# Kernel optimization log

Hardware: AMD Instinct MI355X
Metric: run time of the kernel (lower is better)

Reference implementation:

```python
import jax, jax.numpy as jnp
import numpy as np

E_DIM = 1024
HID = 4096
H = (2 * HID) // 3  # floor(2*hidden/3) = 2730
NUM_EXPERTS = 8
TOP_K = 2
LN_EPS = 1e-5


def setup_inputs() -> dict:
    key = jax.random.key(0)
    ks = jax.random.split(key, 10)
    B, T, P = 2, 8, 256
    s_in = 1.0 / np.sqrt(E_DIM)
    s_h = 1.0 / np.sqrt(H)
    return {
        "x": jax.random.normal(ks[0], (B, T, P, E_DIM), jnp.float32),
        "Wr": jax.random.normal(ks[1], (NUM_EXPERTS, E_DIM), jnp.float32) * s_in,
        "Wv": jax.random.normal(ks[2], (NUM_EXPERTS, E_DIM, H), jnp.float32) * s_in,
        "bv": jax.random.normal(ks[3], (NUM_EXPERTS, H), jnp.float32) * 0.01,
        "Wg": jax.random.normal(ks[4], (NUM_EXPERTS, E_DIM, H), jnp.float32) * s_in,
        "bg": jax.random.normal(ks[5], (NUM_EXPERTS, H), jnp.float32) * 0.01,
        "Wo": jax.random.normal(ks[6], (NUM_EXPERTS, H, E_DIM), jnp.float32) * s_h,
        "bo": jax.random.normal(ks[7], (NUM_EXPERTS, E_DIM), jnp.float32) * 0.01,
        "ln_g": jnp.ones((E_DIM,), jnp.float32),
        "ln_b": jnp.zeros((E_DIM,), jnp.float32),
    }


def reference(x, Wr, Wv, bv, Wg, bg, Wo, bo, ln_g, ln_b):
    B, T, P, E = x.shape
    flat = x.reshape(-1, E)          # [N, E]
    N = flat.shape[0]

    # router: top-k logits -> softmax combine weights
    logits = flat @ Wr.T                              # [N, C]
    tk_vals, tk_idx = jax.lax.top_k(logits, TOP_K)    # [N, K]
    tk_w = jax.nn.softmax(tk_vals, axis=-1)           # [N, K]

    # dense combine-weight matrix: zero for non-routed experts
    comb = jnp.zeros((N, NUM_EXPERTS), flat.dtype)
    comb = comb.at[jnp.arange(N)[:, None], tk_idx].add(tk_w)  # [N, C]

    # all experts over all tokens (masked combine makes this exact)
    hv = jnp.einsum('ne,ceh->cnh', flat, Wv) + bv[:, None, :]  # [C, N, H]
    hg = jnp.einsum('ne,ceh->cnh', flat, Wg) + bg[:, None, :]
    h = jax.nn.silu(hv) * hg                                   # SwiGLU
    oe = jnp.einsum('cnh,che->cne', h, Wo) + bo[:, None, :]    # [C, N, E]
    out = jnp.einsum('cne,nc->ne', oe, comb)                   # weighted combine

    # residual + LayerNorm (AdaptiveNormalizer with no conditioning)
    y = x + out.reshape(B, T, P, E)
    mu = jnp.mean(y, axis=-1, keepdims=True)
    var = jnp.mean((y - mu) ** 2, axis=-1, keepdims=True)
    return ln_g * (y - mu) * jax.lax.rsqrt(var + LN_EPS) + ln_b
```

## Files before the change

kernel.cpp:

```cpp
#include <hip/hip_runtime.h>
#include <hip/hip_bf16.h>

#define E_DIM 1024
#define HDIM  2730
#define HP    2816
#define NEXP  8
#define NTOK  4096
#define NPAIR 8192
#define NSLOT 72
#define LN_EPS 1e-5f

typedef __attribute__((ext_vector_type(8))) short  short8;
typedef __attribute__((ext_vector_type(4))) short  short4v;
typedef __attribute__((ext_vector_type(4))) float  floatx4;
typedef __attribute__((ext_vector_type(4))) int    intx4;

__device__ __forceinline__ __hip_bfloat16 f2bf(float f) { return __float2bfloat16(f); }

__device__ __forceinline__ void gload16(const __hip_bfloat16* g, __hip_bfloat16* l) {
  __builtin_amdgcn_global_load_lds(
      (const __attribute__((address_space(1))) void*)(g),
      (__attribute__((address_space(3))) void*)(l), 16, 0, 0);
}

__global__ __launch_bounds__(256) void router_k(const float* __restrict__ x,
    const float* __restrict__ Wr, int* __restrict__ counts,
    int* __restrict__ tk_idx, float* __restrict__ tk_w) {
  int wid = threadIdx.x >> 6, lane = threadIdx.x & 63;
  int t = blockIdx.x * 4 + wid;
  const float* xr = x + (size_t)t * E_DIM;
  float xv[16];
#pragma unroll
  for (int i = 0; i < 16; ++i) xv[i] = xr[lane + 64 * i];
  float lg[8];
#pragma unroll
  for (int e = 0; e < 8; ++e) {
    const float* wr = Wr + e * E_DIM;
    float a = 0.f;
#pragma unroll
    for (int i = 0; i < 16; ++i) a += xv[i] * wr[lane + 64 * i];
#pragma unroll
    for (int o = 32; o; o >>= 1) a += __shfl_xor(a, o, 64);
    lg[e] = a;
  }
  if (lane == 0) {
    int i0 = 0; float l0 = lg[0];
#pragma unroll
    for (int e = 1; e < 8; ++e) if (lg[e] > l0) { l0 = lg[e]; i0 = e; }
    int i1 = -1; float l1 = -1e30f;
#pragma unroll
    for (int e = 0; e < 8; ++e) if (e != i0 && lg[e] > l1) { l1 = lg[e]; i1 = e; }
    float w0 = 1.f / (1.f + __expf(l1 - l0));
    atomicAdd(&counts[i0], 1);
    atomicAdd(&counts[i1], 1);
    tk_idx[2 * t]     = i0;  tk_idx[2 * t + 1] = i1;
    tk_w[2 * t]       = w0;  tk_w[2 * t + 1]   = 1.f - w0;
  }
}

__global__ void offsets_k(const int* __restrict__ counts, int* __restrict__ offsets,
                          int* __restrict__ cursor,
                          int* __restrict__ slot_e, int* __restrict__ slot_m0) {
  if (threadIdx.x == 0) {
    int off = 0, s = 0;
    for (int e = 0; e < NEXP; ++e) {
      offsets[e] = off; cursor[e] = off;
      for (int m0 = 0; m0 < counts[e]; m0 += 128) { slot_e[s] = e; slot_m0[s] = m0; ++s; }
      off += counts[e];
    }
    for (; s < NSLOT; ++s) { slot_e[s] = -1; slot_m0[s] = 0; }
  }
}

__global__ __launch_bounds__(256) void scatter_k(const int* __restrict__ tk_idx,
    const float* __restrict__ tk_w, int* __restrict__ cursor,
    int* __restrict__ pair_token, float* __restrict__ pair_w, int* __restrict__ pair_pos) {
  int t = blockIdx.x * 256 + threadIdx.x;
#pragma unroll
  for (int k = 0; k < 2; ++k) {
    int e = tk_idx[2 * t + k];
    int pos = atomicAdd(&cursor[e], 1);
    pair_token[pos] = t;
    pair_w[pos] = tk_w[2 * t + k];
    pair_pos[2 * t + k] = pos;
  }
}

__global__ __launch_bounds__(256) void gatherx_k(const float* __restrict__ x,
    const int* __restrict__ pair_token, __hip_bfloat16* __restrict__ xs) {
  int p = blockIdx.x;
  int t = pair_token[p];
  const float* src = x + (size_t)t * E_DIM;
  __hip_bfloat16* dst = xs + (size_t)p * E_DIM;
  int i = threadIdx.x * 4;
  floatx4 v = *(const floatx4*)(src + i);
  union { __hip_bfloat16 h[4]; short4v s; } u;
#pragma unroll
  for (int j = 0; j < 4; ++j) u.h[j] = f2bf(v[j]);
  *(short4v*)(dst + i) = u.s;
}

__global__ __launch_bounds__(256) void tcvt_k(const float* __restrict__ in,
    __hip_bfloat16* __restrict__ out, int R, int C, int outRS,
    size_t inExpStride, size_t outExpStride) {
  __shared__ float tile[64 * 65];
  int e = blockIdx.z;
  const float* ip = in + inExpStride * e;
  __hip_bfloat16* op = out + outExpStride * e;
  int c0 = blockIdx.x * 64, r0 = blockIdx.y * 64;
#pragma unroll
  for (int i = 0; i < 16; ++i) {
    int idx = i * 256 + threadIdx.x;
    int rr = idx >> 6, cc = idx & 63;
    int gr = r0 + rr, gc = c0 + cc;
    tile[rr * 65 + cc] = (gr < R && gc < C) ? ip[(size_t)gr * C + gc] : 0.f;
  }
  __syncthreads();
#pragma unroll
  for (int i = 0; i < 2; ++i) {
    int idx = i * 256 + threadIdx.x;
    int cc = idx >> 3, rb = (idx & 7) * 8;
    union { __hip_bfloat16 h[8]; intx4 v; } u;
#pragma unroll
    for (int j = 0; j < 8; ++j) u.h[j] = f2bf(tile[(rb + j) * 65 + cc]);
    *(intx4*)(op + (size_t)(c0 + cc) * outRS + (r0 + rb)) = u.v;
  }
}

__global__ __launch_bounds__(256, 2) void gemm1_k(
    const __hip_bfloat16* __restrict__ xs,
    const int* __restrict__ counts, const int* __restrict__ offsets,
    const int* __restrict__ slot_e, const int* __restrict__ slot_m0,
    const float* __restrict__ bv, const float* __restrict__ bg,
    const __hip_bfloat16* __restrict__ WvT, const __hip_bfloat16* __restrict__ WgT,
    __hip_bfloat16* __restrict__ h) {
  int slot = blockIdx.y;
  int e = slot_e[slot];
  if (e < 0) return;
  int m0 = slot_m0[slot];
  int Me = counts[e], off = offsets[e];
  int n0 = blockIdx.x * 128;

  __shared__ __align__(16) __hip_bfloat16 sA[128 * 64];
  __shared__ __align__(16) __hip_bfloat16 sBv[128 * 64];
  __shared__ __align__(16) __hip_bfloat16 sBg[128 * 64];

  int tid = threadIdx.x;
  int wid = tid >> 6, lane = tid & 63;
  int wm = wid >> 1, wn = wid & 1;
  int q = lane >> 4, r = lane & 15;
  int key = r & 7;

  int sw[2];
  sw[0] = ((q ^ key) << 3);
  sw[1] = (((4 + q) ^ key) << 3);
  int arow = (wm * 64 + r) * 64;
  int brow = (wn * 64 + r) * 64;

  int srow8  = lane >> 3;
  int schunk = (lane & 7) ^ srow8;
  const __hip_bfloat16* gA0 = xs + (size_t)(off + m0 + wid * 8 + srow8) * E_DIM + schunk * 8;
  size_t wb = (size_t)e * ((size_t)HP * E_DIM);
  size_t browoff = wb + (size_t)(n0 + wid * 8 + srow8) * E_DIM + schunk * 8;
  const __hip_bfloat16* gBv0 = WvT + browoff;
  const __hip_bfloat16* gBg0 = WgT + browoff;
  __hip_bfloat16* lA0  = sA  + wid * 512;
  __hip_bfloat16* lBv0 = sBv + wid * 512;
  __hip_bfloat16* lBg0 = sBg + wid * 512;

  floatx4 accv[4][4], accg[4][4];
  floatx4 zz = {0.f, 0.f, 0.f, 0.f};
#pragma unroll
  for (int mi = 0; mi < 4; ++mi)
#pragma unroll
    for (int ni = 0; ni < 4; ++ni) { accv[mi][ni] = zz; accg[mi][ni] = zz; }

  for (int kt = 0; kt < E_DIM / 64; ++kt) {
    int ko = kt * 64;
#pragma unroll
    for (int i = 0; i < 4; ++i) gload16(gA0  + ko + (size_t)i * 32 * E_DIM, lA0  + i * 2048);
#pragma unroll
    for (int i = 0; i < 4; ++i) gload16(gBv0 + ko + (size_t)i * 32 * E_DIM, lBv0 + i * 2048);
#pragma unroll
    for (int i = 0; i < 4; ++i) gload16(gBg0 + ko + (size_t)i * 32 * E_DIM, lBg0 + i * 2048);
    __syncthreads();
#pragma unroll
    for (int s = 0; s < 2; ++s) {
      short8 av[4];
#pragma unroll
      for (int mi = 0; mi < 4; ++mi)
        av[mi] = *(const short8*)(sA + arow + mi * 16 * 64 + sw[s]);
#pragma unroll
      for (int ni = 0; ni < 4; ++ni) {
        short8 b8v = *(const short8*)(sBv + brow + ni * 16 * 64 + sw[s]);
        short8 b8g = *(const short8*)(sBg + brow + ni * 16 * 64 + sw[s]);
#pragma unroll
        for (int mi = 0; mi < 4; ++mi) {
          accv[mi][ni] = __builtin_amdgcn_mfma_f32_16x16x32_bf16(av[mi], b8v, accv[mi][ni], 0, 0, 0);
          accg[mi][ni] = __builtin_amdgcn_mfma_f32_16x16x32_bf16(av[mi], b8g, accg[mi][ni], 0, 0, 0);
        }
      }
    }
    __syncthreads();
  }

  float bvv[4], bgv[4];
#pragma unroll
  for (int ni = 0; ni < 4; ++ni) {
    int n = n0 + wn * 64 + ni * 16 + r;
    bvv[ni] = (n < HDIM) ? bv[e * HDIM + n] : 0.f;
    bgv[ni] = (n < HDIM) ? bg[e * HDIM + n] : 0.f;
  }
#pragma unroll
  for (int mi = 0; mi < 4; ++mi) {
#pragma unroll
    for (int rr = 0; rr < 4; ++rr) {
      int m_loc = wm * 64 + mi * 16 + q * 4 + rr;
      int m = m0 + m_loc;
      if (m >= Me) continue;
      size_t hrow = (size_t)(off + m) * HP;
#pragma unroll
      for (int ni = 0; ni < 4; ++ni) {
        int n = n0 + wn * 64 + ni * 16 + r;
        float hv = accv[mi][ni][rr] + bvv[ni];
        float hg = accg[mi][ni][rr] + bgv[ni];
        float sgm = 1.f / (1.f + __expf(-hv));
        h[hrow + n] = f2bf(hv * sgm * hg);
      }
    }
  }
}

__global__ __launch_bounds__(256) void gemm2_k(
    const __hip_bfloat16* __restrict__ hb,
    const int* __restrict__ counts, const int* __restrict__ offsets,
    const int* __restrict__ slot_e, const int* __restrict__ slot_m0,
    const float* __restrict__ bo,
    const __hip_bfloat16* __restrict__ WoT,
    float* __restrict__ pout) {
  int slot = blockIdx.y;
  int e = slot_e[slot];
  if (e < 0) return;
  int m0 = slot_m0[slot];
  int Me = counts[e], off = offsets[e];
  int n0 = blockIdx.x * 128;

  __shared__ __align__(16) __hip_bfloat16 sA[128 * 64];
  __shared__ __align__(16) __hip_bfloat16 sB[128 * 64];

  int tid = threadIdx.x;
  int wid = tid >> 6, lane = tid & 63;
  int wm = wid >> 1, wn = wid & 1;
  int q = lane >> 4, r = lane & 15;
  int key = r & 7;

  int sw[2];
  sw[0] = ((q ^ key) << 3);
  sw[1] = (((4 + q) ^ key) << 3);
  int arow = (wm * 64 + r) * 64;
  int brow = (wn * 64 + r) * 64;

  int srow8  = lane >> 3;
  int schunk = (lane & 7) ^ srow8;
  const __hip_bfloat16* gA0 = hb + (size_t)(off + m0 + wid * 8 + srow8) * HP + schunk * 8;
  const __hip_bfloat16* gB0 = WoT + (size_t)e * ((size_t)E_DIM * HP) +
                              (size_t)(n0 + wid * 8 + srow8) * HP + schunk * 8;
  __hip_bfloat16* lA0 = sA + wid * 512;
  __hip_bfloat16* lB0 = sB + wid * 512;

  floatx4 acc[4][4];
  floatx4 zz = {0.f, 0.f, 0.f, 0.f};
#pragma unroll
  for (int mi = 0; mi < 4; ++mi)
#pragma unroll
    for (int ni = 0; ni < 4; ++ni) acc[mi][ni] = zz;

  for (int kt = 0; kt < HP / 64; ++kt) {
    int ko = kt * 64;
#pragma unroll
    for (int i = 0; i < 4; ++i) gload16(gA0 + ko + (size_t)i * 32 * HP, lA0 + i * 2048);
#pragma unroll
    for (int i = 0; i < 4; ++i) gload16(gB0 + ko + (size_t)i * 32 * HP, lB0 + i * 2048);
    __syncthreads();
#pragma unroll
    for (int s = 0; s < 2; ++s) {
      short8 av[4];
#pragma unroll
      for (int mi = 0; mi < 4; ++mi)
        av[mi] = *(const short8*)(sA + arow + mi * 16 * 64 + sw[s]);
#pragma unroll
      for (int ni = 0; ni < 4; ++ni) {
        short8 b8 = *(const short8*)(sB + brow + ni * 16 * 64 + sw[s]);
#pragma unroll
        for (int mi = 0; mi < 4; ++mi)
          acc[mi][ni] = __builtin_amdgcn_mfma_f32_16x16x32_bf16(av[mi], b8, acc[mi][ni], 0, 0, 0);
      }
    }
    __syncthreads();
  }

#pragma unroll
  for (int mi = 0; mi < 4; ++mi) {
#pragma unroll
    for (int rr = 0; rr < 4; ++rr) {
      int m_loc = wm * 64 + mi * 16 + q * 4 + rr;
      int m = m0 + m_loc;
      if (m >= Me) continue;
      size_t orow = (size_t)(off + m) * E_DIM;
#pragma unroll
      for (int ni = 0; ni < 4; ++ni) {
        int n = n0 + wn * 64 + ni * 16 + r;
        pout[orow + n] = acc[mi][ni][rr] + bo[e * E_DIM + n];
      }
    }
  }
}

__global__ __launch_bounds__(256) void ln_k(const float* __restrict__ x,
    const float* __restrict__ pout, const int* __restrict__ pair_pos,
    const float* __restrict__ pair_w, const float* __restrict__ ln_g,
    const float* __restrict__ ln_b, float* __restrict__ out) {
  int t = blockIdx.x, tid = threadIdx.x;
  int p0 = pair_pos[2 * t], p1 = pair_pos[2 * t + 1];
  float w0 = pair_w[p0], w1 = pair_w[p1];
  const float* xr = x + (size_t)t * E_DIM;
  const float* r0 = pout + (size_t)p0 * E_DIM;
  const float* r1 = pout + (size_t)p1 * E_DIM;
  float y[4];
  float s = 0.f, ss = 0.f;
#pragma unroll
  for (int i = 0; i < 4; ++i) {
    int e = tid + 256 * i;
    y[i] = xr[e] + w0 * r0[e] + w1 * r1[e];
    s += y[i];
    ss += y[i] * y[i];
  }
#pragma unroll
  for (int o = 32; o; o >>= 1) { s += __shfl_xor(s, o, 64); ss += __shfl_xor(ss, o, 64); }
  __shared__ float red[8];
  int wid = tid >> 6, lane = tid & 63;
  if (lane == 0) { red[wid] = s; red[4 + wid] = ss; }
  __syncthreads();
  s  = red[0] + red[1] + red[2] + red[3];
  ss = red[4] + red[5] + red[6] + red[7];
  float mu = s * (1.f / E_DIM);
  float var = ss * (1.f / E_DIM) - mu * mu;
  float rs = rsqrtf(var + LN_EPS);
#pragma unroll
  for (int i = 0; i < 4; ++i) {
    int e = tid + 256 * i;
    out[(size_t)t * E_DIM + e] = ln_g[e] * (y[i] - mu) * rs + ln_b[e];
  }
}

extern "C" void kernel_launch(void* const* d_in, const int* in_sizes, int n_in,
                              void* d_out, int out_size, void* d_ws, size_t ws_size,
                              hipStream_t stream) {
  const float* x    = (const float*)d_in[0];
  const float* Wr   = (const float*)d_in[1];
  const float* Wv   = (const float*)d_in[2];
  const float* bv   = (const float*)d_in[3];
  const float* Wg   = (const float*)d_in[4];
  const float* bg   = (const float*)d_in[5];
  const float* Wo   = (const float*)d_in[6];
  const float* bo   = (const float*)d_in[7];
  const float* ln_g = (const float*)d_in[8];
  const float* ln_b = (const float*)d_in[9];
  float* out = (float*)d_out;

  char* ws = (char*)d_ws;
  size_t off = 0;
  auto alloc = [&](size_t bytes) -> void* {
    void* p = ws + off;
    off = (off + bytes + 255) & ~(size_t)255;
    return p;
  };
  int*   counts     = (int*)alloc(32);
  int*   cursor     = (int*)alloc(32);
  int*   offsets    = (int*)alloc(32);
  int*   slot_e     = (int*)alloc(NSLOT * 4);
  int*   slot_m0    = (int*)alloc(NSLOT * 4);
  int*   tk_idx     = (int*)alloc((size_t)NTOK * 2 * 4);
  float* tk_w       = (float*)alloc((size_t)NTOK * 2 * 4);
  int*   pair_token = (int*)alloc((size_t)NPAIR * 4);
  float* pair_w     = (float*)alloc((size_t)NPAIR * 4);
  int*   pair_pos   = (int*)alloc((size_t)NPAIR * 4);
  __hip_bfloat16* xs   = (__hip_bfloat16*)alloc((size_t)(NPAIR + 128) * E_DIM * 2);
  __hip_bfloat16* hbuf = (__hip_bfloat16*)alloc((size_t)(NPAIR + 128) * HP * 2);
  float* pout = (float*)alloc((size_t)NPAIR * E_DIM * 4);

  size_t welems = (size_t)NEXP * HP * E_DIM;
  __hip_bfloat16* WvT = (__hip_bfloat16*)alloc(welems * 2);
  __hip_bfloat16* WgT = (__hip_bfloat16*)alloc(welems * 2);
  __hip_bfloat16* WoT = (__hip_bfloat16*)alloc(welems * 2);

  hipMemsetAsync(d_ws, 0, 1024, stream);

  router_k<<<NTOK / 4, 256, 0, stream>>>(x, Wr, counts, tk_idx, tk_w);
  offsets_k<<<1, 64, 0, stream>>>(counts, offsets, cursor, slot_e, slot_m0);
  scatter_k<<<NTOK / 256, 256, 0, stream>>>(tk_idx, tk_w, cursor, pair_token, pair_w, pair_pos);
  gatherx_k<<<NPAIR, 256, 0, stream>>>(x, pair_token, xs);

  tcvt_k<<<dim3(HP / 64, E_DIM / 64, NEXP), 256, 0, stream>>>(
      Wv, WvT, E_DIM, HDIM, E_DIM, (size_t)E_DIM * HDIM, (size_t)HP * E_DIM);
  tcvt_k<<<dim3(HP / 64, E_DIM / 64, NEXP), 256, 0, stream>>>(
      Wg, WgT, E_DIM, HDIM, E_DIM, (size_t)E_DIM * HDIM, (size_t)HP * E_DIM);
  tcvt_k<<<dim3(E_DIM / 64, HP / 64, NEXP), 256, 0, stream>>>(
      Wo, WoT, HDIM, E_DIM, HP, (size_t)HDIM * E_DIM, (size_t)E_DIM * HP);

  gemm1_k<<<dim3(HP / 128, NSLOT), 256, 0, stream>>>(
      xs, counts, offsets, slot_e, slot_m0, bv, bg, WvT, WgT, hbuf);
  gemm2_k<<<dim3(E_DIM / 128, NSLOT), 256, 0, stream>>>(
      hbuf, counts, offsets, slot_e, slot_m0, bo, WoT, pout);

  ln_k<<<NTOK, 256, 0, stream>>>(x, pout, pair_pos, pair_w, ln_g, ln_b, out);
}
```

Measured before the change: 674.1 us.

## Double-buffer LDS tiles with BK=32 in both expert GEMMs to overlap loads

```diff
diff --git a/kernel.cpp b/kernel.cpp
--- a/kernel.cpp
+++ b/kernel.cpp
@@ -141,32 +141,29 @@
   int Me = counts[e], off = offsets[e];
   int n0 = blockIdx.x * 128;
 
-  __shared__ __align__(16) __hip_bfloat16 sA[128 * 64];
-  __shared__ __align__(16) __hip_bfloat16 sBv[128 * 64];
-  __shared__ __align__(16) __hip_bfloat16 sBg[128 * 64];
+  __shared__ __align__(16) __hip_bfloat16 sA[2][128 * 32];
+  __shared__ __align__(16) __hip_bfloat16 sBv[2][128 * 32];
+  __shared__ __align__(16) __hip_bfloat16 sBg[2][128 * 32];
 
   int tid = threadIdx.x;
   int wid = tid >> 6, lane = tid & 63;
   int wm = wid >> 1, wn = wid & 1;
   int q = lane >> 4, r = lane & 15;
-  int key = r & 7;
-
-  int sw[2];
-  sw[0] = ((q ^ key) << 3);
-  sw[1] = (((4 + q) ^ key) << 3);
-  int arow = (wm * 64 + r) * 64;
-  int brow = (wn * 64 + r) * 64;
-
-  int srow8  = lane >> 3;
-  int schunk = (lane & 7) ^ srow8;
-  const __hip_bfloat16* gA0 = xs + (size_t)(off + m0 + wid * 8 + srow8) * E_DIM + schunk * 8;
+
+  int csw = (q ^ (r & 3)) << 3;
+  int aoff[4], boff[4];
+#pragma unroll
+  for (int mi = 0; mi < 4; ++mi) aoff[mi] = (wm * 64 + mi * 16 + r) * 32 + csw;
+#pragma unroll
+  for (int ni = 0; ni < 4; ++ni) boff[ni] = (wn * 64 + ni * 16 + r) * 32 + csw;
+
+  int srow4   = lane >> 2;
+  int schunk4 = (lane & 3) ^ (srow4 & 3);
+  const __hip_bfloat16* gA = xs + (size_t)(off + m0 + wid * 16 + srow4) * E_DIM + schunk4 * 8;
   size_t wb = (size_t)e * ((size_t)HP * E_DIM);
-  size_t browoff = wb + (size_t)(n0 + wid * 8 + srow8) * E_DIM + schunk * 8;
-  const __hip_bfloat16* gBv0 = WvT + browoff;
-  const __hip_bfloat16* gBg0 = WgT + browoff;
-  __hip_bfloat16* lA0  = sA  + wid * 512;
-  __hip_bfloat16* lBv0 = sBv + wid * 512;
-  __hip_bfloat16* lBg0 = sBg + wid * 512;
+  size_t browoff = wb + (size_t)(n0 + wid * 16 + srow4) * E_DIM + schunk4 * 8;
+  const __hip_bfloat16* gv = WvT + browoff;
+  const __hip_bfloat16* gg = WgT + browoff;
 
   floatx4 accv[4][4], accg[4][4];
   floatx4 zz = {0.f, 0.f, 0.f, 0.f};
@@ -175,34 +172,49 @@
 #pragma unroll
     for (int ni = 0; ni < 4; ++ni) { accv[mi][ni] = zz; accg[mi][ni] = zz; }
 
-  for (int kt = 0; kt < E_DIM / 64; ++kt) {
-    int ko = kt * 64;
-#pragma unroll
-    for (int i = 0; i < 4; ++i) gload16(gA0  + ko + (size_t)i * 32 * E_DIM, lA0  + i * 2048);
-#pragma unroll
-    for (int i = 0; i < 4; ++i) gload16(gBv0 + ko + (size_t)i * 32 * E_DIM, lBv0 + i * 2048);
-#pragma unroll
-    for (int i = 0; i < 4; ++i) gload16(gBg0 + ko + (size_t)i * 32 * E_DIM, lBg0 + i * 2048);
+#define G1_STAGE(BUF)                                                          \
+  {                                                                            \
+    _Pragma("unroll")                                                          \
+    for (int i = 0; i < 2; ++i) {                                              \
+      gload16(gA + (size_t)i * 64 * E_DIM, &sA[BUF][(wid + i * 4) * 512]);     \
+      gload16(gv + (size_t)i * 64 * E_DIM, &sBv[BUF][(wid + i * 4) * 512]);    \
+      gload16(gg + (size_t)i * 64 * E_DIM, &sBg[BUF][(wid + i * 4) * 512]);    \
+    }                                                                          \
+    gA += 32; gv += 32; gg += 32;                                              \
+  }
+
+#define G1_COMPUTE(BUF)                                                        \
+  {                                                                            \
+    short8 av[4];                                                              \
+    _Pragma("unroll")                                                          \
+    for (int mi = 0; mi < 4; ++mi)                                             \
+      av[mi] = *(const short8*)(&sA[BUF][aoff[mi]]);                           \
+    _Pragma("unroll")                                                          \
+    for (int ni = 0; ni < 4; ++ni) {                                           \
+      short8 b8v = *(const short8*)(&sBv[BUF][boff[ni]]);                      \
+      short8 b8g = *(const short8*)(&sBg[BUF][boff[ni]]);                      \
+      _Pragma("unroll")                                                        \
+      for (int mi = 0; mi < 4; ++mi) {                                         \
+        accv[mi][ni] = __builtin_amdgcn_mfma_f32_16x16x32_bf16(av[mi], b8v, accv[mi][ni], 0, 0, 0); \
+        accg[mi][ni] = __builtin_amdgcn_mfma_f32_16x16x32_bf16(av[mi], b8g, accg[mi][ni], 0, 0, 0); \
+      }                                                                        \
+    }                                                                          \
+  }
+
+  G1_STAGE(0);
+  __syncthreads();
+  for (int kt = 0; kt < E_DIM / 32 - 2; kt += 2) {
+    G1_STAGE(1);
+    G1_COMPUTE(0);
     __syncthreads();
-#pragma unroll
-    for (int s = 0; s < 2; ++s) {
-      short8 av[4];
-#pragma unroll
-      for (int mi = 0; mi < 4; ++mi)
-        av[mi] = *(const short8*)(sA + arow + mi * 16 * 64 + sw[s]);
-#pragma unroll
-      for (int ni = 0; ni < 4; ++ni) {
-        short8 b8v = *(const short8*)(sBv + brow + ni * 16 * 64 + sw[s]);
-        short8 b8g = *(const short8*)(sBg + brow + ni * 16 * 64 + sw[s]);
-#pragma unroll
-        for (int mi = 0; mi < 4; ++mi) {
-          accv[mi][ni] = __builtin_amdgcn_mfma_f32_16x16x32_bf16(av[mi], b8v, accv[mi][ni], 0, 0, 0);
-          accg[mi][ni] = __builtin_amdgcn_mfma_f32_16x16x32_bf16(av[mi], b8g, accg[mi][ni], 0, 0, 0);
-        }
-      }
-    }
+    G1_STAGE(0);
+    G1_COMPUTE(1);
     __syncthreads();
   }
+  G1_STAGE(1);
+  G1_COMPUTE(0);
+  __syncthreads();
+  G1_COMPUTE(1);
 
   float bvv[4], bgv[4];
 #pragma unroll
@@ -231,7 +243,7 @@
   }
 }
 
-__global__ __launch_bounds__(256) void gemm2_k(
+__global__ __launch_bounds__(256, 2) void gemm2_k(
     const __hip_bfloat16* __restrict__ hb,
     const int* __restrict__ counts, const int* __restrict__ offsets,
     const int* __restrict__ slot_e, const int* __restrict__ slot_m0,
@@ -245,28 +257,26 @@
   int Me = counts[e], off = offsets[e];
   int n0 = blockIdx.x * 128;
 
-  __shared__ __align__(16) __hip_bfloat16 sA[128 * 64];
-  __shared__ __align__(16) __hip_bfloat16 sB[128 * 64];
+  __shared__ __align__(16) __hip_bfloat16 sA[2][128 * 32];
+  __shared__ __align__(16) __hip_bfloat16 sB[2][128 * 32];
 
   int tid = threadIdx.x;
   int wid = tid >> 6, lane = tid & 63;
   int wm = wid >> 1, wn = wid & 1;
   int q = lane >> 4, r = lane & 15;
-  int key = r & 7;
-
-  int sw[2];
-  sw[0] = ((q ^ key) << 3);
-  sw[1] = (((4 + q) ^ key) << 3);
-  int arow = (wm * 64 + r) * 64;
-  int brow = (wn * 64 + r) * 64;
-
-  int srow8  = lane >> 3;
-  int schunk = (lane & 7) ^ srow8;
-  const __hip_bfloat16* gA0 = hb + (size_t)(off + m0 + wid * 8 + srow8) * HP + schunk * 8;
-  const __hip_bfloat16* gB0 = WoT + (size_t)e * ((size_t)E_DIM * HP) +
-                              (size_t)(n0 + wid * 8 + srow8) * HP + schunk * 8;
-  __hip_bfloat16* lA0 = sA + wid * 512;
-  __hip_bfloat16* lB0 = sB + wid * 512;
+
+  int csw = (q ^ (r & 3)) << 3;
+  int aoff[4], boff[4];
+#pragma unroll
+  for (int mi = 0; mi < 4; ++mi) aoff[mi] = (wm * 64 + mi * 16 + r) * 32 + csw;
+#pragma unroll
+  for (int ni = 0; ni < 4; ++ni) boff[ni] = (wn * 64 + ni * 16 + r) * 32 + csw;
+
+  int srow4   = lane >> 2;
+  int schunk4 = (lane & 3) ^ (srow4 & 3);
+  const __hip_bfloat16* gA = hb + (size_t)(off + m0 + wid * 16 + srow4) * HP + schunk4 * 8;
+  const __hip_bfloat16* gB = WoT + (size_t)e * ((size_t)E_DIM * HP) +
+                             (size_t)(n0 + wid * 16 + srow4) * HP + schunk4 * 8;
 
   floatx4 acc[4][4];
   floatx4 zz = {0.f, 0.f, 0.f, 0.f};
@@ -275,29 +285,45 @@
 #pragma unroll
     for (int ni = 0; ni < 4; ++ni) acc[mi][ni] = zz;
 
-  for (int kt = 0; kt < HP / 64; ++kt) {
-    int ko = kt * 64;
-#pragma unroll
-    for (int i = 0; i < 4; ++i) gload16(gA0 + ko + (size_t)i * 32 * HP, lA0 + i * 2048);
-#pragma unroll
-    for (int i = 0; i < 4; ++i) gload16(gB0 + ko + (size_t)i * 32 * HP, lB0 + i * 2048);
+#define G2_STAGE(BUF)                                                          \
+  {                                                                            \
+    _Pragma("unroll")                                                          \
+    for (int i = 0; i < 2; ++i) {                                              \
+      gload16(gA + (size_t)i * 64 * HP, &sA[BUF][(wid + i * 4) * 512]);        \
+      gload16(gB + (size_t)i * 64 * HP, &sB[BUF][(wid + i * 4) * 512]);        \
+    }                                                                          \
+    gA += 32; gB += 32;                                                        \
+  }
+
+#define G2_COMPUTE(BUF)                                                        \
+  {                                                                            \
+    short8 av[4];                                                              \
+    _Pragma("unroll")                                                          \
+    for (int mi = 0; mi < 4; ++mi)                                             \
+      av[mi] = *(const short8*)(&sA[BUF][aoff[mi]]);                           \
+    _Pragma("unroll")                                                          \
+    for (int ni = 0; ni < 4; ++ni) {                                           \
+      short8 b8 = *(const short8*)(&sB[BUF][boff[ni]]);                        \
+      _Pragma("unroll")                                                        \
+      for (int mi = 0; mi < 4; ++mi)                                           \
+        acc[mi][ni] = __builtin_amdgcn_mfma_f32_16x16x32_bf16(av[mi], b8, acc[mi][ni], 0, 0, 0); \
+    }                                                                          \
+  }
+
+  G2_STAGE(0);
+  __syncthreads();
+  for (int kt = 0; kt < HP / 32 - 2; kt += 2) {
+    G2_STAGE(1);
+    G2_COMPUTE(0);
     __syncthreads();
-#pragma unroll
-    for (int s = 0; s < 2; ++s) {
-      short8 av[4];
-#pragma unroll
-      for (int mi = 0; mi < 4; ++mi)
-        av[mi] = *(const short8*)(sA + arow + mi * 16 * 64 + sw[s]);
-#pragma unroll
-      for (int ni = 0; ni < 4; ++ni) {
-        short8 b8 = *(const short8*)(sB + brow + ni * 16 * 64 + sw[s]);
-#pragma unroll
-        for (int mi = 0; mi < 4; ++mi)
-          acc[mi][ni] = __builtin_amdgcn_mfma_f32_16x16x32_bf16(av[mi], b8, acc[mi][ni], 0, 0, 0);
-      }
-    }
+    G2_STAGE(0);
+    G2_COMPUTE(1);
     __syncthreads();
   }
+  G2_STAGE(1);
+  G2_COMPUTE(0);
+  __syncthreads();
+  G2_COMPUTE(1);
 
 #pragma unroll
   for (int mi = 0; mi < 4; ++mi) {
```

Result: slower. 731.9 us (+8.6%).
